# Performance work log

Measured on AMD Instinct MI355X. Metric: run time of the kernel, lower is better.

The kernel has to match this reference:

```python
import jax, jax.numpy as jnp
import numpy as np

N, E = 100000, 1600000
NODE_IN, EDGE_IN, H = 128, 16, 128


def sage_conv(x, src, dst, Wl, Wr, b, n_nodes):
    # PyG SAGEConv (aggr='mean'): out = lin_l(mean_{j->i} x_j) + lin_r(x_i), bias on lin_l
    msg_sum = jax.ops.segment_sum(x[src], dst, num_segments=n_nodes)      # [N, d]
    cnt = jax.ops.segment_sum(jnp.ones((src.shape[0],), x.dtype), dst, num_segments=n_nodes)
    mean = msg_sum / jnp.maximum(cnt, 1.0)[:, None]                        # empty neighborhoods -> 0
    return mean @ Wl + x @ Wr + b


def setup_inputs() -> dict:
    key = jax.random.key(0)
    ks = jax.random.split(key, 12)
    s = lambda d: 1.0 / np.sqrt(d)
    return {
        "x": jax.random.normal(ks[0], (N, NODE_IN), jnp.float32),
        "edge_index": jax.random.randint(ks[1], (2, E), 0, N, dtype=jnp.int64),
        "edge_attr": jax.random.normal(ks[2], (E, EDGE_IN), jnp.float32),
        "Wl1": jax.random.normal(ks[3], (NODE_IN, H), jnp.float32) * s(NODE_IN),
        "Wr1": jax.random.normal(ks[4], (NODE_IN, H), jnp.float32) * s(NODE_IN),
        "b1": jnp.zeros((H,), jnp.float32),
        "Wl2": jax.random.normal(ks[5], (H, H), jnp.float32) * s(H),
        "Wr2": jax.random.normal(ks[6], (H, H), jnp.float32) * s(H),
        "b2": jnp.zeros((H,), jnp.float32),
        "Wm1": jax.random.normal(ks[7], (2 * H + EDGE_IN, H), jnp.float32) * s(2 * H + EDGE_IN),
        "bm1": jnp.zeros((H,), jnp.float32),
        "Wm2": jax.random.normal(ks[8], (H, 1), jnp.float32) * s(H),
        "bm2": jnp.zeros((1,), jnp.float32),
    }


def reference(x, edge_index, edge_attr, Wl1, Wr1, b1, Wl2, Wr2, b2, Wm1, bm1, Wm2, bm2):
    src, dst = edge_index[0], edge_index[1]
    h = jax.nn.relu(sage_conv(x, src, dst, Wl1, Wr1, b1, N))
    h = jax.nn.relu(sage_conv(h, src, dst, Wl2, Wr2, b2, N))
    edge_feat = jnp.concatenate([h[src], h[dst], edge_attr], axis=1)  # [E, 2H+edge_in]
    out = jax.nn.relu(edge_feat @ Wm1 + bm1) @ Wm2 + bm2               # dropout is identity in eval
    return out.reshape(-1)
```

## Files before the change

kernel.cpp:

```cpp
#include <hip/hip_runtime.h>

typedef _Float16 f16;
typedef _Float16 f16x2 __attribute__((ext_vector_type(2)));
typedef _Float16 f16x8 __attribute__((ext_vector_type(8)));
typedef float f32x4 __attribute__((ext_vector_type(4)));

#define MFMA16(a,b,c) __builtin_amdgcn_mfma_f32_16x16x32_f16((a),(b),(c),0,0,0)

__global__ void k_detect(const long long* ei, int n_nodes, int* flag) {
    long long v = ei[threadIdx.x];
    int bad = (v < 0 || v >= n_nodes);
    unsigned long long m = __ballot(bad);
    if (threadIdx.x == 0) *flag = (m == 0ULL);
}

__global__ void k_idx(const void* ei, int E, const int* __restrict__ flag,
                      int* __restrict__ src, int* __restrict__ dst,
                      int* __restrict__ deg) {
    int e = blockIdx.x * 256 + threadIdx.x;
    if (e >= E) return;
    int s, d;
    if (*flag) {
        const long long* p = (const long long*)ei;
        s = (int)p[e];
        d = (int)p[(size_t)E + e];
    } else {
        const int* p = (const int*)ei;
        s = p[e];
        d = p[(size_t)E + e];
    }
    src[e] = s;
    dst[e] = d;
    atomicAdd(&deg[d], 1);
}

__global__ void k_x2h(const float* __restrict__ x, f16* __restrict__ xh, int n) {
    int i = (blockIdx.x * 256 + threadIdx.x) * 8;
    if (i >= n) return;
    float4 a = *(const float4*)(x + i);
    float4 b = *(const float4*)(x + i + 4);
    f16x8 h;
    h[0] = (f16)a.x; h[1] = (f16)a.y; h[2] = (f16)a.z; h[3] = (f16)a.w;
    h[4] = (f16)b.x; h[5] = (f16)b.y; h[6] = (f16)b.z; h[7] = (f16)b.w;
    *(f16x8*)(xh + i) = h;
}

__global__ void k_wfrag(const float* __restrict__ Wa, const float* __restrict__ Wb,
                        f16* __restrict__ dst, int KS) {
    int t = blockIdx.x * 256 + threadIdx.x;
    int total = KS * 8 * 64;
    if (t >= total) return;
    int l = t & 63;
    int s = t >> 9;
    int k0 = s * 32 + (l >> 4) * 8;
    int j = ((t >> 6) & 7) * 16 + (l & 15);
    f16x8 h;
    #pragma unroll
    for (int e = 0; e < 8; e++) {
        int k = k0 + e;
        float v = (k < 128) ? Wa[k * 128 + j] : Wb[(k - 128) * 128 + j];
        h[e] = (f16)v;
    }
    *(f16x8*)(dst + (size_t)t * 8) = h;
}

__global__ void k_zfrag(const float* __restrict__ Wm1, f16* __restrict__ dst) {
    int t = blockIdx.x * 256 + threadIdx.x;
    if (t >= 4 * 16 * 64) return;
    int lane = t & 63, c = (t >> 6) & 15, s = t >> 10;
    int k0 = s * 32 + (lane >> 4) * 8;
    int j = c * 16 + (lane & 15);
    f16x8 h;
    #pragma unroll
    for (int e = 0; e < 8; e++) {
        int k = k0 + e;
        float v = (j < 128) ? Wm1[k * 128 + j] : Wm1[(128 + k) * 128 + (j - 128)];
        h[e] = (f16)v;
    }
    *(f16x8*)(dst + (size_t)t * 8) = h;
}

__global__ void k_wefrag(const float* __restrict__ Wm1, f16* __restrict__ dst) {
    int t = blockIdx.x * 256 + threadIdx.x;
    if (t >= 8 * 64) return;
    int lane = t & 63, ct = t >> 6;
    int k0 = (lane >> 4) * 8;
    int j = (ct >> 1) * 32 + 2 * (lane & 15) + (ct & 1);
    f16x8 h;
    #pragma unroll
    for (int e = 0; e < 8; e++) {
        int k = k0 + e;
        h[e] = (k < 16) ? (f16)Wm1[(256 + k) * 128 + j] : (f16)0.0f;
    }
    *(f16x8*)(dst + (size_t)t * 8) = h;
}

__global__ void k_bsum(const int* __restrict__ deg, int n, int* __restrict__ bsum) {
    __shared__ int ws[4];
    const int tid = threadIdx.x;
    int i = blockIdx.x * 1024 + tid * 4;
    int s = 0;
    if (i + 3 < n) {
        int4 d = *(const int4*)(deg + i);
        s = d.x + d.y + d.z + d.w;
    } else {
        #pragma unroll
        for (int j = 0; j < 4; j++) if (i + j < n) s += deg[i + j];
    }
    #pragma unroll
    for (int m = 1; m < 64; m <<= 1) s += __shfl_xor(s, m, 64);
    if ((tid & 63) == 0) ws[tid >> 6] = s;
    __syncthreads();
    if (tid == 0) bsum[blockIdx.x] = ws[0] + ws[1] + ws[2] + ws[3];
}

__global__ void k_bscan(int* __restrict__ bsum, int nb, int* __restrict__ rowptr_n) {
    __shared__ int wsum[4];
    const int tid = threadIdx.x, lane = tid & 63, wid = tid >> 6;
    int v = (tid < nb) ? bsum[tid] : 0;
    int inc = v;
    #pragma unroll
    for (int off = 1; off < 64; off <<= 1) {
        int u = __shfl_up(inc, off, 64);
        if (lane >= off) inc += u;
    }
    if (lane == 63) wsum[wid] = inc;
    __syncthreads();
    int woff = 0;
    for (int j = 0; j < wid; j++) woff += wsum[j];
    int excl = woff + inc - v;
    if (tid < nb) bsum[tid] = excl;
    if (tid == nb - 1) rowptr_n[0] = excl + v;
}

__global__ void k_rowptr(const int* __restrict__ deg, int n, const int* __restrict__ boff,
                         int* __restrict__ rowptr, int* __restrict__ cursor) {
    __shared__ int wsum[4];
    const int tid = threadIdx.x, lane = tid & 63, wid = tid >> 6;
    int i = blockIdx.x * 1024 + tid * 4;
    int d0 = 0, d1 = 0, d2 = 0, d3 = 0;
    if (i + 3 < n) {
        int4 d = *(const int4*)(deg + i);
        d0 = d.x; d1 = d.y; d2 = d.z; d3 = d.w;
    } else {
        if (i     < n) d0 = deg[i];
        if (i + 1 < n) d1 = deg[i + 1];
        if (i + 2 < n) d2 = deg[i + 2];
        if (i + 3 < n) d3 = deg[i + 3];
    }
    int s = d0 + d1 + d2 + d3;
    int inc = s;
    #pragma unroll
    for (int off = 1; off < 64; off <<= 1) {
        int u = __shfl_up(inc, off, 64);
        if (lane >= off) inc += u;
    }
    if (lane == 63) wsum[wid] = inc;
    __syncthreads();
    int woff = 0;
    for (int j = 0; j < wid; j++) woff += wsum[j];
    int excl = boff[blockIdx.x] + woff + inc - s;
    int e1 = excl + d0, e2 = e1 + d1, e3 = e2 + d2;
    if (i     < n) { rowptr[i]     = excl; cursor[i]     = excl; }
    if (i + 1 < n) { rowptr[i + 1] = e1;   cursor[i + 1] = e1; }
    if (i + 2 < n) { rowptr[i + 2] = e2;   cursor[i + 2] = e2; }
    if (i + 3 < n) { rowptr[i + 3] = e3;   cursor[i + 3] = e3; }
}

__global__ void k_scatter(const int* __restrict__ src, const int* __restrict__ dst, int E,
                          int* __restrict__ cursor, int* __restrict__ col,
                          int* __restrict__ eid, int* __restrict__ dstp) {
    int e = blockIdx.x * 256 + threadIdx.x;
    if (e < E) {
        int d = dst[e];
        int p = atomicAdd(&cursor[d], 1);
        col[p] = src[e];
        eid[p] = e;
        dstp[p] = d;
    }
}

#define AP 136
template<int DO_Z>
__global__ __launch_bounds__(256, DO_Z ? 4 : 5) void k_fuse(
    const f16* __restrict__ tab,
    const int* __restrict__ rowptr, const int* __restrict__ col,
    const f16* __restrict__ Wf, const float* __restrict__ bias,
    const f16* __restrict__ zwf, const float* __restrict__ bm1,
    f16* __restrict__ out, int n_rows) {
    __shared__ __align__(16) f16 sA[64 * AP];
    const int tid = threadIdx.x, lane = tid & 63, w = tid >> 6;
    const int l15 = lane & 15, g = lane >> 4;
    const int base = blockIdx.x * 64;

    const int g16 = tid >> 4, c = tid & 15;
    #pragma unroll
    for (int rep = 0; rep < 4; rep++) {
        const int node = base + rep * 16 + g16;
        float acc[8] = {0.f, 0.f, 0.f, 0.f, 0.f, 0.f, 0.f, 0.f};
        int d = 1;
        if (node < n_rows) {
            const int s0 = rowptr[node], s1 = rowptr[node + 1];
            int k = s0;
            for (; k + 3 < s1; k += 4) {
                const int n0 = col[k], n1 = col[k + 1], n2 = col[k + 2], n3 = col[k + 3];
                f16x8 v0 = *(const f16x8*)(tab + (size_t)n0 * 128 + c * 8);
                f16x8 v1 = *(const f16x8*)(tab + (size_t)n1 * 128 + c * 8);
                f16x8 v2 = *(const f16x8*)(tab + (size_t)n2 * 128 + c * 8);
                f16x8 v3 = *(const f16x8*)(tab + (size_t)n3 * 128 + c * 8);
                #pragma unroll
                for (int j = 0; j < 8; j++)
                    acc[j] += ((float)v0[j] + (float)v1[j]) + ((float)v2[j] + (float)v3[j]);
            }
            for (; k < s1; ++k) {
                const int n0 = col[k];
                f16x8 v0 = *(const f16x8*)(tab + (size_t)n0 * 128 + c * 8);
                #pragma unroll
                for (int j = 0; j < 8; j++) acc[j] += (float)v0[j];
            }
            d = s1 - s0; if (d < 1) d = 1;
        }
        const float inv = 1.f / (float)d;
        f16x8 r;
        #pragma unroll
        for (int j = 0; j < 8; j++) r[j] = (f16)(acc[j] * inv);
        *(f16x8*)&sA[(rep * 16 + g16) * AP + c * 8] = r;
    }
    __syncthreads();

    const int c0 = (2 * w) * 16 + l15, c1 = c0 + 16;
    const float b0 = bias[c0], b1 = bias[c1];
    f32x4 acc[4][2];
    #pragma unroll
    for (int t = 0; t < 4; t++) {
        acc[t][0] = f32x4{b0, b0, b0, b0};
        acc[t][1] = f32x4{b1, b1, b1, b1};
    }
    #pragma unroll
    for (int s = 0; s < 8; s++) {
        f16x8 bf0 = *(const f16x8*)&Wf[((size_t)(s * 8 + 2 * w    ) * 64 + lane) * 8];
        f16x8 bf1 = *(const f16x8*)&Wf[((size_t)(s * 8 + 2 * w + 1) * 64 + lane) * 8];
        const int koff = (s & 3) * 32 + g * 8;
        #pragma unroll
        for (int t = 0; t < 4; t++) {
            f16x8 a;
            if (s < 4) {
                a = *(const f16x8*)&sA[(t * 16 + l15) * AP + koff];
            } else {
                int row = base + t * 16 + l15;
                if (row >= n_rows) row = n_rows - 1;
                a = *(const f16x8*)(tab + (size_t)row * 128 + koff);
            }
            acc[t][0] = MFMA16(a, bf0, acc[t][0]);
            acc[t][1] = MFMA16(a, bf1, acc[t][1]);
        }
    }

    if (DO_Z == 0) {
        #pragma unroll
        for (int t = 0; t < 4; t++) {
            #pragma unroll
            for (int i = 0; i < 4; i++) {
                int row = base + t * 16 + g * 4 + i;
                if (row < n_rows) {
                    float v0 = acc[t][0][i]; v0 = v0 > 0.f ? v0 : 0.f;
                    float v1 = acc[t][1][i]; v1 = v1 > 0.f ? v1 : 0.f;
                    out[(size_t)row * 128 + c0] = (f16)v0;
                    out[(size_t)row * 128 + c1] = (f16)v1;
                }
            }
        }
    } else {
        __syncthreads();
        #pragma unroll
        for (int t = 0; t < 4; t++) {
            #pragma unroll
            for (int i = 0; i < 4; i++) {
                const int rl = t * 16 + g * 4 + i;
                float v0 = acc[t][0][i]; v0 = v0 > 0.f ? v0 : 0.f;
                float v1 = acc[t][1][i]; v1 = v1 > 0.f ? v1 : 0.f;
                sA[rl * AP + c0] = (f16)v0;
                sA[rl * AP + c1] = (f16)v1;
            }
        }
        __syncthreads();
        #pragma unroll
        for (int half = 0; half < 2; half++) {
            const int j0 = (4 * w + 2 * half) * 16 + l15, j1 = j0 + 16;
            const float zb0 = (j0 >= 128) ? bm1[j0 - 128] : 0.0f;
            const float zb1 = (j1 >= 128) ? bm1[j1 - 128] : 0.0f;
            f32x4 zacc[4][2];
            #pragma unroll
            for (int t = 0; t < 4; t++) {
                zacc[t][0] = f32x4{zb0, zb0, zb0, zb0};
                zacc[t][1] = f32x4{zb1, zb1, zb1, zb1};
            }
            #pragma unroll
            for (int s = 0; s < 4; s++) {
                f16x8 wf0 = *(const f16x8*)&zwf[((size_t)(s * 16 + 4 * w + 2 * half    ) * 64 + lane) * 8];
                f16x8 wf1 = *(const f16x8*)&zwf[((size_t)(s * 16 + 4 * w + 2 * half + 1) * 64 + lane) * 8];
                const int koff = s * 32 + g * 8;
                #pragma unroll
                for (int t = 0; t < 4; t++) {
                    f16x8 a = *(const f16x8*)&sA[(t * 16 + l15) * AP + koff];
                    zacc[t][0] = MFMA16(a, wf0, zacc[t][0]);
                    zacc[t][1] = MFMA16(a, wf1, zacc[t][1]);
                }
            }
            #pragma unroll
            for (int t = 0; t < 4; t++) {
                #pragma unroll
                for (int i = 0; i < 4; i++) {
                    int row = base + t * 16 + g * 4 + i;
                    if (row < n_rows) {
                        out[(size_t)row * 256 + j0] = (f16)zacc[t][0][i];
                        out[(size_t)row * 256 + j1] = (f16)zacc[t][1][i];
                    }
                }
            }
        }
    }
}

#define ZP3 136
__global__ __launch_bounds__(256, 4) void k_edge3(
    const f16* __restrict__ z, const float* __restrict__ ea,
    const int* __restrict__ colp, const int* __restrict__ dstp, const int* __restrict__ eidp,
    const f16* __restrict__ wef, const float* __restrict__ Wm2,
    const float* __restrict__ bm2, float* __restrict__ tmp,
    int E, int iters, int nwaves) {
    __shared__ __align__(16) f16 sZ[4][16 * ZP3];
    const int tid = threadIdx.x, lane = tid & 63, w = tid >> 6;
    const int l15 = lane & 15, g = lane >> 4;
    const int te = lane >> 2, sq = lane & 3;
    const int gw = blockIdx.x * 4 + w;

    f16x8 be[8];
    #pragma unroll
    for (int cc = 0; cc < 8; cc++)
        be[cc] = *(const f16x8*)(wef + ((size_t)(cc * 64 + lane)) * 8);
    float2 w2p[4];
    #pragma unroll
    for (int pg = 0; pg < 4; pg++)
        w2p[pg] = *(const float2*)&Wm2[pg * 32 + 2 * l15];
    const float bv = bm2[0];

    f16* myZ = &sZ[w][0];

    f16x8 zs[4], zd[4];
    f16x8 a_cur, a_next;

    auto stage_load = [&](int pbase, f16x8* zsv, f16x8* zdv, f16x8& av) {
        int pr = pbase + te; if (pr > E - 1) pr = E - 1;
        const int is = colp[pr], id = dstp[pr];
        const f16* ps = z + (size_t)is * 256 + sq * 8;
        const f16* pd = z + (size_t)id * 256 + 128 + sq * 8;
        #pragma unroll
        for (int i = 0; i < 4; i++) {
            zsv[i] = *(const f16x8*)(ps + i * 32);
            zdv[i] = *(const f16x8*)(pd + i * 32);
        }
        int pe = pbase + l15; if (pe > E - 1) pe = E - 1;
        f16x8 av_ = {};
        if (g < 2) {
            const int ee = eidp[pe];
            float4 e0 = *(const float4*)(ea + (size_t)ee * 16 + g * 8);
            float4 e1 = *(const float4*)(ea + (size_t)ee * 16 + g * 8 + 4);
            av_[0] = (f16)e0.x; av_[1] = (f16)e0.y; av_[2] = (f16)e0.z; av_[3] = (f16)e0.w;
            av_[4] = (f16)e1.x; av_[5] = (f16)e1.y; av_[6] = (f16)e1.z; av_[7] = (f16)e1.w;
        }
        av = av_;
    };
    auto stage_write = [&]() {
        f16* zp = myZ + te * ZP3 + sq * 8;
        #pragma unroll
        for (int i = 0; i < 4; i++) {
            f16x8 v = zs[i] + zd[i];
            *(f16x8*)(zp + i * 32) = v;
        }
    };

    stage_load(gw * 16, zs, zd, a_cur);
    stage_write();

    for (int it = 0; it < iters; ++it) {
        const int pbase = (gw + it * nwaves) * 16;
        if (pbase >= E) break;
        const int nxt = (gw + (it + 1) * nwaves) * 16;
        const bool has_next = (it + 1 < iters) && (nxt < E);
        if (has_next) stage_load(nxt, zs, zd, a_next);

        f32x4 acc[8];
        #pragma unroll
        for (int cc = 0; cc < 8; cc++) acc[cc] = f32x4{0.f, 0.f, 0.f, 0.f};
        #pragma unroll
        for (int cc = 0; cc < 8; cc++) acc[cc] = MFMA16(a_cur, be[cc], acc[cc]);

        float p[4];
        #pragma unroll
        for (int i = 0; i < 4; i++) {
            const int edge = g * 4 + i;
            float s = 0.f;
            #pragma unroll
            for (int pg = 0; pg < 4; pg++) {
                f16x2 zz = *(const f16x2*)&myZ[edge * ZP3 + pg * 32 + 2 * l15];
                float v0 = (float)zz[0] + acc[2 * pg    ][i]; v0 = v0 > 0.f ? v0 : 0.f;
                float v1 = (float)zz[1] + acc[2 * pg + 1][i]; v1 = v1 > 0.f ? v1 : 0.f;
                s += v0 * w2p[pg].x + v1 * w2p[pg].y;
            }
            p[i] = s;
        }
        #pragma unroll
        for (int m = 1; m < 16; m <<= 1)
            #pragma unroll
            for (int i = 0; i < 4; i++) p[i] += __shfl_xor(p[i], m, 64);
        if (l15 == 0) {
            #pragma unroll
            for (int i = 0; i < 4; i++) {
                int pp = pbase + g * 4 + i;
                if (pp < E) tmp[pp] = p[i] + bv;
            }
        }
        if (has_next) {
            stage_write();
            a_cur = a_next;
        }
    }
}

__global__ void k_perm(const float* __restrict__ tmp, const int* __restrict__ eidp,
                       float* __restrict__ out, int E) {
    int p = blockIdx.x * 256 + threadIdx.x;
    if (p < E) out[eidp[p]] = tmp[p];
}

extern "C" void kernel_launch(void* const* d_in, const int* in_sizes, int n_in,
                              void* d_out, int out_size, void* d_ws, size_t ws_size,
                              hipStream_t stream) {
    const float* x   = (const float*)d_in[0];
    const void*  ei  = d_in[1];
    const float* ea  = (const float*)d_in[2];
    const float* Wl1 = (const float*)d_in[3];
    const float* Wr1 = (const float*)d_in[4];
    const float* b1  = (const float*)d_in[5];
    const float* Wl2 = (const float*)d_in[6];
    const float* Wr2 = (const float*)d_in[7];
    const float* b2  = (const float*)d_in[8];
    const float* Wm1 = (const float*)d_in[9];
    const float* bm1 = (const float*)d_in[10];
    const float* Wm2 = (const float*)d_in[11];
    const float* bm2 = (const float*)d_in[12];

    const int N = in_sizes[0] / 128;
    const int E = in_sizes[1] / 2;

    char* ws = (char*)d_ws;
    size_t off = 0;
    auto alloc = [&](size_t bytes) -> void* {
        void* p = ws + off;
        off = (off + bytes + 255) & ~(size_t)255;
        return p;
    };
    f16* z      = (f16*)alloc((size_t)N * 256 * 2);
    f16* xh     = z;
    f16* h1     = (f16*)alloc((size_t)N * 128 * 2);
    int* src    = (int*)alloc((size_t)E * 4);
    int* dst    = (int*)alloc((size_t)E * 4);
    int* col    = (int*)alloc((size_t)E * 4);
    int* eid    = (int*)alloc((size_t)E * 4);
    int* dstp   = (int*)alloc((size_t)E * 4);
    float* tmp  = (float*)alloc((size_t)E * 4);
    int* deg    = (int*)alloc((size_t)N * 4);
    int* rowptr = (int*)alloc((size_t)(N + 1) * 4);
    int* cursor = (int*)alloc((size_t)N * 4);
    int* bsum   = (int*)alloc((size_t)1024 * 4);
    f16* w1f    = (f16*)alloc((size_t)8 * 8 * 64 * 8 * 2);
    f16* w2f    = (f16*)alloc((size_t)8 * 8 * 64 * 8 * 2);
    f16* zwf    = (f16*)alloc((size_t)4 * 16 * 64 * 8 * 2);
    f16* wef    = (f16*)alloc((size_t)8 * 64 * 8 * 2);
    int* flag   = (int*)alloc(4);
    if (off > ws_size) return;

    const int eb = (E + 255) / 256;
    const int nbk = (N + 1023) / 1024;
    const int rb64 = (N + 63) / 64;

    k_detect<<<1, 64, 0, stream>>>((const long long*)ei, N, flag);
    hipMemsetAsync(deg, 0, (size_t)N * 4, stream);
    k_idx<<<eb, 256, 0, stream>>>(ei, E, flag, src, dst, deg);
    k_x2h<<<(N * 128 / 8 + 255) / 256, 256, 0, stream>>>(x, xh, N * 128);
    k_wfrag<<<16, 256, 0, stream>>>(Wl1, Wr1, w1f, 8);
    k_wfrag<<<16, 256, 0, stream>>>(Wl2, Wr2, w2f, 8);
    k_zfrag<<<16, 256, 0, stream>>>(Wm1, zwf);
    k_wefrag<<<2, 256, 0, stream>>>(Wm1, wef);

    k_bsum<<<nbk, 256, 0, stream>>>(deg, N, bsum);
    k_bscan<<<1, 256, 0, stream>>>(bsum, nbk, rowptr + N);
    k_rowptr<<<nbk, 256, 0, stream>>>(deg, N, bsum, rowptr, cursor);
    k_scatter<<<eb, 256, 0, stream>>>(src, dst, E, cursor, col, eid, dstp);

    k_fuse<0><<<rb64, 256, 0, stream>>>(xh, rowptr, col, w1f, b1, nullptr, nullptr, h1, N);
    k_fuse<1><<<rb64, 256, 0, stream>>>(h1, rowptr, col, w2f, b2, zwf, bm1, z, N);

    const int eg = 1792;
    const int nwaves = eg * 4;
    const int ntiles = (E + 15) / 16;
    const int e_iters = (ntiles + nwaves - 1) / nwaves;
    k_edge3<<<eg, 256, 0, stream>>>(z, ea, col, dstp, eid, wef, Wm2, bm2,
                                    tmp, E, e_iters, nwaves);
    k_perm<<<eb, 256, 0, stream>>>(tmp, eid, (float*)d_out, E);
}
```

Measured before the change: 502.6 us.

## Merge prep kernels, pack edge metadata, write edge outputs directly, drop permute

Merges the x-to-half conversion and the four weight-fragment kernels into a single prep launch. Packs src, edge id and dst into one int4 per sorted edge so the edge kernel does one vector load instead of separate gathers. The edge kernel now writes each result straight to its original edge position via a shuffled edge id, which removes the tmp buffer and the permute kernel. The edge grid also grows from 1792 to 2048 blocks. In exchange, the output stores become scattered and the packed array takes more bytes per edge to write in scatter.

```diff
diff --git a/kernel.cpp b/kernel.cpp
--- a/kernel.cpp
+++ b/kernel.cpp
@@ -34,22 +34,8 @@
     atomicAdd(&deg[d], 1);
 }
 
-__global__ void k_x2h(const float* __restrict__ x, f16* __restrict__ xh, int n) {
-    int i = (blockIdx.x * 256 + threadIdx.x) * 8;
-    if (i >= n) return;
-    float4 a = *(const float4*)(x + i);
-    float4 b = *(const float4*)(x + i + 4);
-    f16x8 h;
-    h[0] = (f16)a.x; h[1] = (f16)a.y; h[2] = (f16)a.z; h[3] = (f16)a.w;
-    h[4] = (f16)b.x; h[5] = (f16)b.y; h[6] = (f16)b.z; h[7] = (f16)b.w;
-    *(f16x8*)(xh + i) = h;
-}
-
-__global__ void k_wfrag(const float* __restrict__ Wa, const float* __restrict__ Wb,
-                        f16* __restrict__ dst, int KS) {
-    int t = blockIdx.x * 256 + threadIdx.x;
-    int total = KS * 8 * 64;
-    if (t >= total) return;
+__device__ __forceinline__ void wfrag_body(const float* Wa, const float* Wb,
+                                           f16* dst, int t) {
     int l = t & 63;
     int s = t >> 9;
     int k0 = s * 32 + (l >> 4) * 8;
@@ -64,35 +50,63 @@
     *(f16x8*)(dst + (size_t)t * 8) = h;
 }
 
-__global__ void k_zfrag(const float* __restrict__ Wm1, f16* __restrict__ dst) {
-    int t = blockIdx.x * 256 + threadIdx.x;
-    if (t >= 4 * 16 * 64) return;
-    int lane = t & 63, c = (t >> 6) & 15, s = t >> 10;
-    int k0 = s * 32 + (lane >> 4) * 8;
-    int j = c * 16 + (lane & 15);
-    f16x8 h;
-    #pragma unroll
-    for (int e = 0; e < 8; e++) {
-        int k = k0 + e;
-        float v = (j < 128) ? Wm1[k * 128 + j] : Wm1[(128 + k) * 128 + (j - 128)];
-        h[e] = (f16)v;
-    }
-    *(f16x8*)(dst + (size_t)t * 8) = h;
-}
-
-__global__ void k_wefrag(const float* __restrict__ Wm1, f16* __restrict__ dst) {
-    int t = blockIdx.x * 256 + threadIdx.x;
-    if (t >= 8 * 64) return;
-    int lane = t & 63, ct = t >> 6;
-    int k0 = (lane >> 4) * 8;
-    int j = (ct >> 1) * 32 + 2 * (lane & 15) + (ct & 1);
-    f16x8 h;
-    #pragma unroll
-    for (int e = 0; e < 8; e++) {
-        int k = k0 + e;
-        h[e] = (k < 16) ? (f16)Wm1[(256 + k) * 128 + j] : (f16)0.0f;
-    }
-    *(f16x8*)(dst + (size_t)t * 8) = h;
+__global__ void k_prep(const float* __restrict__ x,
+                       const float* __restrict__ Wl1, const float* __restrict__ Wr1,
+                       const float* __restrict__ Wl2, const float* __restrict__ Wr2,
+                       const float* __restrict__ Wm1,
+                       f16* __restrict__ xh, f16* __restrict__ w1f, f16* __restrict__ w2f,
+                       f16* __restrict__ zwf, f16* __restrict__ wef, int N) {
+    const int xb = (N * 16 + 255) / 256;
+    int b = blockIdx.x;
+    if (b < xb) {
+        int i = (b * 256 + threadIdx.x) * 8;
+        if (i >= N * 128) return;
+        float4 a = *(const float4*)(x + i);
+        float4 c = *(const float4*)(x + i + 4);
+        f16x8 h;
+        h[0] = (f16)a.x; h[1] = (f16)a.y; h[2] = (f16)a.z; h[3] = (f16)a.w;
+        h[4] = (f16)c.x; h[5] = (f16)c.y; h[6] = (f16)c.z; h[7] = (f16)c.w;
+        *(f16x8*)(xh + i) = h;
+        return;
+    }
+    b -= xb;
+    if (b < 16) {
+        wfrag_body(Wl1, Wr1, w1f, b * 256 + threadIdx.x);
+        return;
+    }
+    if (b < 32) {
+        wfrag_body(Wl2, Wr2, w2f, (b - 16) * 256 + threadIdx.x);
+        return;
+    }
+    if (b < 48) {
+        int t = (b - 32) * 256 + threadIdx.x;
+        int lane = t & 63, c = (t >> 6) & 15, s = t >> 10;
+        int k0 = s * 32 + (lane >> 4) * 8;
+        int j = c * 16 + (lane & 15);
+        f16x8 h;
+        #pragma unroll
+        for (int e = 0; e < 8; e++) {
+            int k = k0 + e;
+            float v = (j < 128) ? Wm1[k * 128 + j] : Wm1[(128 + k) * 128 + (j - 128)];
+            h[e] = (f16)v;
+        }
+        *(f16x8*)(zwf + (size_t)t * 8) = h;
+        return;
+    }
+    {
+        int t = (b - 48) * 256 + threadIdx.x;
+        if (t >= 8 * 64) return;
+        int lane = t & 63, ct = t >> 6;
+        int k0 = (lane >> 4) * 8;
+        int j = (ct >> 1) * 32 + 2 * (lane & 15) + (ct & 1);
+        f16x8 h;
+        #pragma unroll
+        for (int e = 0; e < 8; e++) {
+            int k = k0 + e;
+            h[e] = (k < 16) ? (f16)Wm1[(256 + k) * 128 + j] : (f16)0.0f;
+        }
+        *(f16x8*)(wef + (size_t)t * 8) = h;
+    }
 }
 
 __global__ void k_bsum(const int* __restrict__ deg, int n, int* __restrict__ bsum) {
@@ -169,14 +183,13 @@
 
 __global__ void k_scatter(const int* __restrict__ src, const int* __restrict__ dst, int E,
                           int* __restrict__ cursor, int* __restrict__ col,
-                          int* __restrict__ eid, int* __restrict__ dstp) {
+                          int4* __restrict__ pk) {
     int e = blockIdx.x * 256 + threadIdx.x;
     if (e < E) {
-        int d = dst[e];
+        int s = src[e], d = dst[e];
         int p = atomicAdd(&cursor[d], 1);
-        col[p] = src[e];
-        eid[p] = e;
-        dstp[p] = d;
+        col[p] = s;
+        pk[p] = make_int4(s, e, d, 0);
     }
 }
 
@@ -325,9 +338,9 @@
 #define ZP3 136
 __global__ __launch_bounds__(256, 4) void k_edge3(
     const f16* __restrict__ z, const float* __restrict__ ea,
-    const int* __restrict__ colp, const int* __restrict__ dstp, const int* __restrict__ eidp,
+    const int4* __restrict__ pk,
     const f16* __restrict__ wef, const float* __restrict__ Wm2,
-    const float* __restrict__ bm2, float* __restrict__ tmp,
+    const float* __restrict__ bm2, float* __restrict__ out,
     int E, int iters, int nwaves) {
     __shared__ __align__(16) f16 sZ[4][16 * ZP3];
     const int tid = threadIdx.x, lane = tid & 63, w = tid >> 6;
@@ -349,10 +362,13 @@
 
     f16x8 zs[4], zd[4];
     f16x8 a_cur, a_next;
-
-    auto stage_load = [&](int pbase, f16x8* zsv, f16x8* zdv, f16x8& av) {
+    int eid_cur, eid_next;
+
+    auto stage_load = [&](int pbase, f16x8* zsv, f16x8* zdv, f16x8& av, int& eidv) {
         int pr = pbase + te; if (pr > E - 1) pr = E - 1;
-        const int is = colp[pr], id = dstp[pr];
+        const int4 v = pk[pr];
+        const int is = v.x, ee = v.y, id = v.z;
+        eidv = ee;
         const f16* ps = z + (size_t)is * 256 + sq * 8;
         const f16* pd = z + (size_t)id * 256 + 128 + sq * 8;
         #pragma unroll
@@ -363,9 +379,9 @@
         int pe = pbase + l15; if (pe > E - 1) pe = E - 1;
         f16x8 av_ = {};
         if (g < 2) {
-            const int ee = eidp[pe];
-            float4 e0 = *(const float4*)(ea + (size_t)ee * 16 + g * 8);
-            float4 e1 = *(const float4*)(ea + (size_t)ee * 16 + g * 8 + 4);
+            const int ee2 = pk[pe].y;
+            float4 e0 = *(const float4*)(ea + (size_t)ee2 * 16 + g * 8);
+            float4 e1 = *(const float4*)(ea + (size_t)ee2 * 16 + g * 8 + 4);
             av_[0] = (f16)e0.x; av_[1] = (f16)e0.y; av_[2] = (f16)e0.z; av_[3] = (f16)e0.w;
             av_[4] = (f16)e1.x; av_[5] = (f16)e1.y; av_[6] = (f16)e1.z; av_[7] = (f16)e1.w;
         }
@@ -380,7 +396,7 @@
         }
     };
 
-    stage_load(gw * 16, zs, zd, a_cur);
+    stage_load(gw * 16, zs, zd, a_cur, eid_cur);
     stage_write();
 
     for (int it = 0; it < iters; ++it) {
@@ -388,7 +404,7 @@
         if (pbase >= E) break;
         const int nxt = (gw + (it + 1) * nwaves) * 16;
         const bool has_next = (it + 1 < iters) && (nxt < E);
-        if (has_next) stage_load(nxt, zs, zd, a_next);
+        if (has_next) stage_load(nxt, zs, zd, a_next, eid_next);
 
         f32x4 acc[8];
         #pragma unroll
@@ -414,24 +430,21 @@
         for (int m = 1; m < 16; m <<= 1)
             #pragma unroll
             for (int i = 0; i < 4; i++) p[i] += __shfl_xor(p[i], m, 64);
-        if (l15 == 0) {
-            #pragma unroll
-            for (int i = 0; i < 4; i++) {
+        #pragma unroll
+        for (int i = 0; i < 4; i++) {
+            int esrc = (lane & 48) + 4 * i;
+            int ei_ = __shfl(eid_cur, esrc, 64);
+            if (l15 == 0) {
                 int pp = pbase + g * 4 + i;
-                if (pp < E) tmp[pp] = p[i] + bv;
+                if (pp < E) out[ei_] = p[i] + bv;
             }
         }
         if (has_next) {
             stage_write();
             a_cur = a_next;
-        }
-    }
-}
-
-__global__ void k_perm(const float* __restrict__ tmp, const int* __restrict__ eidp,
-                       float* __restrict__ out, int E) {
-    int p = blockIdx.x * 256 + threadIdx.x;
-    if (p < E) out[eidp[p]] = tmp[p];
+            eid_cur = eid_next;
+        }
+    }
 }
 
 extern "C" void kernel_launch(void* const* d_in, const int* in_sizes, int n_in,
@@ -467,9 +480,7 @@
     int* src    = (int*)alloc((size_t)E * 4);
     int* dst    = (int*)alloc((size_t)E * 4);
     int* col    = (int*)alloc((size_t)E * 4);
-    int* eid    = (int*)alloc((size_t)E * 4);
-    int* dstp   = (int*)alloc((size_t)E * 4);
-    float* tmp  = (float*)alloc((size_t)E * 4);
+    int4* pk    = (int4*)alloc((size_t)E * 16);
     int* deg    = (int*)alloc((size_t)N * 4);
     int* rowptr = (int*)alloc((size_t)(N + 1) * 4);
     int* cursor = (int*)alloc((size_t)N * 4);
@@ -488,25 +499,22 @@
     k_detect<<<1, 64, 0, stream>>>((const long long*)ei, N, flag);
     hipMemsetAsync(deg, 0, (size_t)N * 4, stream);
     k_idx<<<eb, 256, 0, stream>>>(ei, E, flag, src, dst, deg);
-    k_x2h<<<(N * 128 / 8 + 255) / 256, 256, 0, stream>>>(x, xh, N * 128);
-    k_wfrag<<<16, 256, 0, stream>>>(Wl1, Wr1, w1f, 8);
-    k_wfrag<<<16, 256, 0, stream>>>(Wl2, Wr2, w2f, 8);
-    k_zfrag<<<16, 256, 0, stream>>>(Wm1, zwf);
-    k_wefrag<<<2, 256, 0, stream>>>(Wm1, wef);
+    const int xb = (N * 16 + 255) / 256;
+    k_prep<<<xb + 50, 256, 0, stream>>>(x, Wl1, Wr1, Wl2, Wr2, Wm1,
+                                        xh, w1f, w2f, zwf, wef, N);
 
     k_bsum<<<nbk, 256, 0, stream>>>(deg, N, bsum);
     k_bscan<<<1, 256, 0, stream>>>(bsum, nbk, rowptr + N);
     k_rowptr<<<nbk, 256, 0, stream>>>(deg, N, bsum, rowptr, cursor);
-    k_scatter<<<eb, 256, 0, stream>>>(src, dst, E, cursor, col, eid, dstp);
+    k_scatter<<<eb, 256, 0, stream>>>(src, dst, E, cursor, col, pk);
 
     k_fuse<0><<<rb64, 256, 0, stream>>>(xh, rowptr, col, w1f, b1, nullptr, nullptr, h1, N);
     k_fuse<1><<<rb64, 256, 0, stream>>>(h1, rowptr, col, w2f, b2, zwf, bm1, z, N);
 
-    const int eg = 1792;
+    const int eg = 2048;
     const int nwaves = eg * 4;
     const int ntiles = (E + 15) / 16;
     const int e_iters = (ntiles + nwaves - 1) / nwaves;
-    k_edge3<<<eg, 256, 0, stream>>>(z, ea, col, dstp, eid, wef, Wm2, bm2,
-                                    tmp, E, e_iters, nwaves);
-    k_perm<<<eb, 256, 0, stream>>>(tmp, eid, (float*)d_out, E);
-}
+    k_edge3<<<eg, 256, 0, stream>>>(z, ea, pk, wef, Wm2, bm2,
+                                    (float*)d_out, E, e_iters, nwaves);
+}
```

Result: slower. 530.1 us (+5.5%).
